# Kernel optimization log

Hardware: AMD Instinct MI355X
Metric: run time of the kernel (lower is better)

Reference implementation:

```python
import jax, jax.numpy as jnp
import numpy as np

N = 50000      # total nodes (actors) across batch
E = 300000     # edges surviving the distance threshold
N_AGT = 128    # n_actor
N_CTX = 128    # n_ctx == n_actor for A2A
EPS = 1e-5


def _gn(x, gamma, beta):
    # torch GroupNorm(num_groups=1) on a [N, C] tensor: normalize over C per row
    mu = jnp.mean(x, axis=-1, keepdims=True)
    var = jnp.mean((x - mu) ** 2, axis=-1, keepdims=True)
    return (x - mu) * jax.lax.rsqrt(var + EPS) * gamma + beta


def setup_inputs() -> dict:
    key = jax.random.key(0)
    ks = jax.random.split(key, 16)
    s = 0.02
    f32 = jnp.float32
    inp = {
        'agts': jax.random.normal(ks[0], (N, N_AGT), f32),
        'ctx': jax.random.normal(ks[1], (N, N_CTX), f32),
        'agt_ctrs': jax.random.normal(ks[2], (N, 2), f32),
        'ctx_ctrs': jax.random.normal(ks[3], (N, 2), f32),
        'hi': jax.random.randint(ks[4], (E,), 0, N, dtype=jnp.int32),
        'wi': jax.random.randint(ks[5], (E,), 0, N, dtype=jnp.int32),
        # dist: nn.Linear(2, n_ctx) -> ReLU -> Linear(n_ctx, n_ctx, GN, act)
        'w_d1': jax.random.normal(ks[6], (N_CTX, 2), f32) * s,
        'b_d1': jnp.zeros((N_CTX,), f32),
        'w_d2': jax.random.normal(ks[7], (N_CTX, N_CTX), f32) * s,
        'g_d2': jnp.ones((N_CTX,), f32), 'bt_d2': jnp.zeros((N_CTX,), f32),
        # query: Linear(n_agt, n_ctx, GN, act)
        'w_q': jax.random.normal(ks[8], (N_CTX, N_AGT), f32) * s,
        'g_q': jnp.ones((N_CTX,), f32), 'bt_q': jnp.zeros((N_CTX,), f32),
        # ctx: Linear(3*n_ctx, n_agt, GN, act) -> nn.Linear(n_agt, n_agt, bias=False)
        'w_c1': jax.random.normal(ks[9], (N_AGT, 3 * N_CTX), f32) * s,
        'g_c1': jnp.ones((N_AGT,), f32), 'bt_c1': jnp.zeros((N_AGT,), f32),
        'w_c2': jax.random.normal(ks[10], (N_AGT, N_AGT), f32) * s,
        # agt: nn.Linear(n_agt, n_agt, bias=False)
        'w_a': jax.random.normal(ks[11], (N_AGT, N_AGT), f32) * s,
        # norm: GroupNorm(1, n_agt)
        'g_n': jnp.ones((N_AGT,), f32), 'bt_n': jnp.zeros((N_AGT,), f32),
        # linear: Linear(n_agt, n_agt, GN, act=False)
        'w_l': jax.random.normal(ks[12], (N_AGT, N_AGT), f32) * s,
        'g_l': jnp.ones((N_AGT,), f32), 'bt_l': jnp.zeros((N_AGT,), f32),
    }
    return inp


def reference(agts, ctx, agt_ctrs, ctx_ctrs, hi, wi,
              w_d1, b_d1, w_d2, g_d2, bt_d2,
              w_q, g_q, bt_q,
              w_c1, g_c1, bt_c1, w_c2,
              w_a, g_n, bt_n,
              w_l, g_l, bt_l):
    res = agts
    # edge-wise distance features: [E, 2] -> [E, n_ctx]
    d = agt_ctrs[hi] - ctx_ctrs[wi]
    d = jax.nn.relu(d @ w_d1.T + b_d1)
    d = jax.nn.relu(_gn(d @ w_d2.T, g_d2, bt_d2))
    # edge-wise query from gathered target nodes: [E, n_ctx]
    q = jax.nn.relu(_gn(agts[hi] @ w_q.T, g_q, bt_q))
    # fuse dist/query/context: [E, 3*n_ctx] -> [E, n_agt]
    e = jnp.concatenate([d, q, ctx[wi]], axis=-1)
    e = jax.nn.relu(_gn(e @ w_c1.T, g_c1, bt_c1))
    e = e @ w_c2.T
    # scatter-add messages back to nodes
    out = agts @ w_a.T
    out = out.at[hi].add(e)
    out = jax.nn.relu(_gn(out, g_n, bt_n))
    out = _gn(out @ w_l.T, g_l, bt_l)
    return jax.nn.relu(out + res)
```

## Files before the change

### kernel.cpp

```cpp
#include <hip/hip_runtime.h>
#include <hip/hip_bf16.h>

#define NCH 128
#define EB  64
#define NB  32

typedef __attribute__((ext_vector_type(8))) short bf16x8;
typedef __attribute__((ext_vector_type(4))) float f32x4;

__device__ inline unsigned short f2bf(float v) {
    __hip_bfloat16 h = __float2bfloat16(v);
    return __builtin_bit_cast(unsigned short, h);
}
__device__ inline float bf2f(unsigned short u) {
    return __builtin_bit_cast(float, (unsigned int)u << 16);
}

__device__ inline bf16x8 cvt8(const float* __restrict__ p) {
    bf16x8 r;
#pragma unroll
    for (int i = 0; i < 8; ++i) r[i] = (short)f2bf(p[i]);
    return r;
}

template<bool BF>
__device__ inline bf16x8 load_row8(const void* __restrict__ src, int node, int koff) {
    if constexpr (BF)
        return *(const bf16x8*)((const unsigned short*)src + (size_t)node * NCH + koff);
    else
        return cvt8((const float*)src + (size_t)node * NCH + koff);
}

__global__ __launch_bounds__(256) void convert_weights_kernel(
    const float* __restrict__ w_d2, const float* __restrict__ w_q,
    const float* __restrict__ w_c1, const float* __restrict__ w_c2,
    const float* __restrict__ w_a,  const float* __restrict__ w_l,
    unsigned short* __restrict__ out)
{
    int i = blockIdx.x * 256 + threadIdx.x;
    if (i >= 131072) return;
    const float* src; int off;
    if      (i < 16384)  { src = w_d2; off = i; }
    else if (i < 32768)  { src = w_q;  off = i - 16384; }
    else if (i < 49152)  { int j = i - 32768; src = w_c1; off = (j >> 7) * 384 + (j & 127); }
    else if (i < 65536)  { int j = i - 49152; src = w_c1; off = (j >> 7) * 384 + 128 + (j & 127); }
    else if (i < 81920)  { int j = i - 65536; src = w_c1; off = (j >> 7) * 384 + 256 + (j & 127); }
    else if (i < 98304)  { src = w_c2; off = i - 81920; }
    else if (i < 114688) { src = w_a;  off = i - 98304; }
    else                 { src = w_l;  off = i - 114688; }
    out[i] = f2bf(src[off]);
}

__device__ inline void gemm_k128_lds(const unsigned short* __restrict__ A,
                                     const unsigned short* __restrict__ W,
                                     int lane, int wave, f32x4 (&acc)[2][2])
{
#pragma unroll
    for (int k = 0; k < 4; ++k) {
        const int koff = k * 32 + (lane >> 4) * 8;
        bf16x8 a[2], b[2];
#pragma unroll
        for (int m = 0; m < 2; ++m) {
            int r = m * 16 + (lane & 15);
            int byte = (r * 256 + koff * 2) ^ ((r & 7) << 4);
            a[m] = *(const bf16x8*)((const char*)A + byte);
        }
#pragma unroll
        for (int n = 0; n < 2; ++n) {
            int wr = wave * 32 + n * 16 + (lane & 15);
            b[n] = *(const bf16x8*)(W + (size_t)wr * NCH + koff);
        }
#pragma unroll
        for (int m = 0; m < 2; ++m)
#pragma unroll
            for (int n = 0; n < 2; ++n)
                acc[m][n] = __builtin_amdgcn_mfma_f32_16x16x32_bf16(a[m], b[n], acc[m][n], 0, 0, 0);
    }
}

__device__ inline void gemm_k128_dual(const unsigned short* __restrict__ A,
                                      const unsigned short* __restrict__ W,
                                      int lane, int wave,
                                      f32x4 (&accA)[2][2], f32x4 (&accB)[2][2])
{
#pragma unroll
    for (int k = 0; k < 4; ++k) {
        const int koff = k * 32 + (lane >> 4) * 8;
        bf16x8 b[2];
#pragma unroll
        for (int n = 0; n < 2; ++n) {
            int wr = wave * 32 + n * 16 + (lane & 15);
            b[n] = *(const bf16x8*)(W + (size_t)wr * NCH + koff);
        }
        bf16x8 a0[2], a1[2];
#pragma unroll
        for (int m = 0; m < 2; ++m) {
            int r = m * 16 + (lane & 15);
            a0[m] = *(const bf16x8*)((const char*)A + ((r * 256 + koff * 2) ^ ((r & 7) << 4)));
            int r2 = r + 32;
            a1[m] = *(const bf16x8*)((const char*)A + ((r2 * 256 + koff * 2) ^ ((r2 & 7) << 4)));
        }
#pragma unroll
        for (int m = 0; m < 2; ++m)
#pragma unroll
            for (int n = 0; n < 2; ++n) {
                accA[m][n] = __builtin_amdgcn_mfma_f32_16x16x32_bf16(a0[m], b[n], accA[m][n], 0, 0, 0);
                accB[m][n] = __builtin_amdgcn_mfma_f32_16x16x32_bf16(a1[m], b[n], accB[m][n], 0, 0, 0);
            }
    }
}

__device__ inline void gn_stats_half(const f32x4 (&acc)[2][2],
                                     float (*red_s)[4], float (*red_q)[4],
                                     int lane, int wave, int roff)
{
#pragma unroll
    for (int m = 0; m < 2; ++m)
#pragma unroll
        for (int j = 0; j < 4; ++j) {
            float sv = acc[m][0][j] + acc[m][1][j];
            float qv = acc[m][0][j] * acc[m][0][j] + acc[m][1][j] * acc[m][1][j];
#pragma unroll
            for (int off = 1; off < 16; off <<= 1) {
                sv += __shfl_xor(sv, off);
                qv += __shfl_xor(qv, off);
            }
            if ((lane & 15) == 0) {
                int r = roff + m * 16 + (lane >> 4) * 4 + j;
                red_s[r][wave] = sv;
                red_q[r][wave] = qv;
            }
        }
}

__device__ inline void gn_apply_half(const f32x4 (&acc)[2][2],
                                     float (*red_s)[4], float (*red_q)[4],
                                     const float* __restrict__ gamma,
                                     const float* __restrict__ beta,
                                     unsigned short* __restrict__ dst,
                                     int lane, int wave, int roff)
{
    const int c0 = wave * 32 + (lane & 15);
    const float g0 = gamma[c0],      b0 = beta[c0];
    const float g1 = gamma[c0 + 16], b1 = beta[c0 + 16];
#pragma unroll
    for (int m = 0; m < 2; ++m)
#pragma unroll
        for (int j = 0; j < 4; ++j) {
            int r = roff + m * 16 + ((lane >> 4) << 2) + j;
            float4 sv = *(const float4*)red_s[r];
            float4 qv = *(const float4*)red_q[r];
            float ssum = (sv.x + sv.y) + (sv.z + sv.w);
            float qsum = (qv.x + qv.y) + (qv.z + qv.w);
            float mu  = ssum * (1.f / NCH);
            float var = qsum * (1.f / NCH) - mu * mu;
            float rs  = rsqrtf(var + 1e-5f);
            float v0 = fmaxf((acc[m][0][j] - mu) * rs * g0 + b0, 0.f);
            float v1 = fmaxf((acc[m][1][j] - mu) * rs * g1 + b1, 0.f);
            unsigned int p0 = f2bf(v0), p1 = f2bf(v1);
            unsigned int o0 = (unsigned int)__shfl_xor((int)p0, 1);
            unsigned int o1 = (unsigned int)__shfl_xor((int)p1, 1);
            if (!(lane & 1)) {
                int cb = c0 * 2;
                int byte0 = (r * 256 + cb) ^ ((r & 7) << 4);
                int byte1 = (r * 256 + cb + 32) ^ ((r & 7) << 4);
                *(unsigned int*)((char*)dst + byte0) = (p0 & 0xffffu) | (o0 << 16);
                *(unsigned int*)((char*)dst + byte1) = (p1 & 0xffffu) | (o1 << 16);
            }
        }
}

__device__ inline void scatter_half(const f32x4 (&acc)[2][2], const int* __restrict__ sh_h,
                                    float* __restrict__ outbuf, int e0, int E,
                                    int lane, int wave, int roff)
{
#pragma unroll
    for (int m = 0; m < 2; ++m)
#pragma unroll
        for (int n = 0; n < 2; ++n)
#pragma unroll
            for (int j = 0; j < 4; ++j) {
                int r = roff + m * 16 + ((lane >> 4) << 2) + j;
                if (e0 + r < E)
                    atomicAdd(&outbuf[(size_t)sh_h[r] * NCH + wave * 32 + n * 16 + (lane & 15)],
                              acc[m][n][j]);
            }
}

__device__ inline void gn_frag_stats(const f32x4 (&acc)[2][2],
                                     float (*red_s)[4], float (*red_q)[4],
                                     int t, float (&mu)[2][4], float (&rs)[2][4])
{
    const int lane = t & 63, wave = t >> 6;
    gn_stats_half(acc, red_s, red_q, lane, wave, 0);
    __syncthreads();
#pragma unroll
    for (int m = 0; m < 2; ++m)
#pragma unroll
        for (int j = 0; j < 4; ++j) {
            int r = m * 16 + ((lane >> 4) << 2) + j;
            float4 sv = *(const float4*)red_s[r];
            float4 qv = *(const float4*)red_q[r];
            float ssum = (sv.x + sv.y) + (sv.z + sv.w);
            float qsum = (qv.x + qv.y) + (qv.z + qv.w);
            float m_  = ssum * (1.f / NCH);
            float var = qsum * (1.f / NCH) - m_ * m_;
            mu[m][j] = m_;
            rs[m][j] = rsqrtf(var + 1e-5f);
        }
}

__device__ inline void gn_pack_store(const f32x4 (&acc)[2][2],
                                     const float (&mu)[2][4], const float (&rs)[2][4],
                                     const float* __restrict__ gamma,
                                     const float* __restrict__ beta,
                                     unsigned short* __restrict__ dst, int t)
{
    const int lane = t & 63, wave = t >> 6;
    const int c0 = wave * 32 + (lane & 15);
    const float g0 = gamma[c0],      b0 = beta[c0];
    const float g1 = gamma[c0 + 16], b1 = beta[c0 + 16];
#pragma unroll
    for (int m = 0; m < 2; ++m)
#pragma unroll
        for (int j = 0; j < 4; ++j) {
            int r = m * 16 + ((lane >> 4) << 2) + j;
            float v0 = fmaxf((acc[m][0][j] - mu[m][j]) * rs[m][j] * g0 + b0, 0.f);
            float v1 = fmaxf((acc[m][1][j] - mu[m][j]) * rs[m][j] * g1 + b1, 0.f);
            unsigned int p0 = f2bf(v0), p1 = f2bf(v1);
            unsigned int o0 = (unsigned int)__shfl_xor((int)p0, 1);
            unsigned int o1 = (unsigned int)__shfl_xor((int)p1, 1);
            if (!(lane & 1)) {
                int cb = c0 * 2;
                int byte0 = (r * 256 + cb) ^ ((r & 7) << 4);
                int byte1 = (r * 256 + cb + 32) ^ ((r & 7) << 4);
                *(unsigned int*)((char*)dst + byte0) = (p0 & 0xffffu) | (o0 << 16);
                *(unsigned int*)((char*)dst + byte1) = (p1 & 0xffffu) | (o1 << 16);
            }
        }
    __syncthreads();
}

__device__ inline void frag_pack_global(const f32x4 (&acc)[2][2],
                                        unsigned short* __restrict__ dst,
                                        int n0, int N, int t)
{
    const int lane = t & 63, wave = t >> 6;
    const int c0 = wave * 32 + (lane & 15);
#pragma unroll
    for (int m = 0; m < 2; ++m)
#pragma unroll
        for (int j = 0; j < 4; ++j) {
            int r = m * 16 + ((lane >> 4) << 2) + j;
            int ng = n0 + r;
            unsigned int p0 = f2bf(acc[m][0][j]);
            unsigned int p1 = f2bf(acc[m][1][j]);
            unsigned int o0 = (unsigned int)__shfl_xor((int)p0, 1);
            unsigned int o1 = (unsigned int)__shfl_xor((int)p1, 1);
            if (!(lane & 1) && ng < N) {
                unsigned int* rowp = (unsigned int*)(dst + (size_t)ng * NCH);
                rowp[c0 >> 1]        = (p0 & 0xffffu) | (o0 << 16);
                rowp[(c0 + 16) >> 1] = (p1 & 0xffffu) | (o1 << 16);
            }
        }
}

__global__ __launch_bounds__(256) void node_prep_kernel(
    const float* __restrict__ agts, const float* __restrict__ ctx,
    const unsigned short* __restrict__ wbf,
    const float* __restrict__ g_q, const float* __restrict__ bt_q,
    float* __restrict__ outbuf,
    unsigned short* __restrict__ pq, unsigned short* __restrict__ px, int N)
{
    const int t = threadIdx.x;
    const int lane = t & 63, wave = t >> 6;
    const int n0 = blockIdx.x * NB;

    __shared__ unsigned short bfQ[NB * NCH];
    __shared__ __align__(16) float red_s[NB][4];
    __shared__ __align__(16) float red_q[NB][4];

    const unsigned short* Wq   = wbf + 16384;
    const unsigned short* Wc1q = wbf + 49152;
    const unsigned short* Wc1x = wbf + 65536;
    const unsigned short* Wa   = wbf + 98304;

    int r0 = n0 + (lane & 15);      if (r0 >= N) r0 = N - 1;
    int r1 = n0 + 16 + (lane & 15); if (r1 >= N) r1 = N - 1;

    const f32x4 z = { 0.f, 0.f, 0.f, 0.f };
    f32x4 accO[2][2] = { { z, z }, { z, z } };
    f32x4 accQ[2][2] = { { z, z }, { z, z } };
#pragma unroll
    for (int k = 0; k < 4; ++k) {
        const int koff = k * 32 + (lane >> 4) * 8;
        bf16x8 a[2], bo[2], bq[2];
        a[0] = load_row8<false>(agts, r0, koff);
        a[1] = load_row8<false>(agts, r1, koff);
#pragma unroll
        for (int n = 0; n < 2; ++n) {
            int wr = wave * 32 + n * 16 + (lane & 15);
            bo[n] = *(const bf16x8*)(Wa + (size_t)wr * NCH + koff);
            bq[n] = *(const bf16x8*)(Wq + (size_t)wr * NCH + koff);
        }
#pragma unroll
        for (int m = 0; m < 2; ++m)
#pragma unroll
            for (int n = 0; n < 2; ++n) {
                accO[m][n] = __builtin_amdgcn_mfma_f32_16x16x32_bf16(a[m], bo[n], accO[m][n], 0, 0, 0);
                accQ[m][n] = __builtin_amdgcn_mfma_f32_16x16x32_bf16(a[m], bq[n], accQ[m][n], 0, 0, 0);
            }
    }
#pragma unroll
    for (int m = 0; m < 2; ++m)
#pragma unroll
        for (int n = 0; n < 2; ++n)
#pragma unroll
            for (int j = 0; j < 4; ++j) {
                int r = m * 16 + ((lane >> 4) << 2) + j;
                int ng = n0 + r;
                if (ng < N)
                    outbuf[(size_t)ng * NCH + wave * 32 + n * 16 + (lane & 15)] = accO[m][n][j];
            }
    float mu[2][4], rs[2][4];
    gn_frag_stats(accQ, red_s, red_q, t, mu, rs);
    gn_pack_store(accQ, mu, rs, g_q, bt_q, bfQ, t);

    f32x4 accPq[2][2] = { { z, z }, { z, z } };
    f32x4 accPx[2][2] = { { z, z }, { z, z } };
#pragma unroll
    for (int k = 0; k < 4; ++k) {
        const int koff = k * 32 + (lane >> 4) * 8;
        bf16x8 aq[2], ax[2], bq2[2], bx[2];
#pragma unroll
        for (int m = 0; m < 2; ++m) {
            int r = m * 16 + (lane & 15);
            int byte = (r * 256 + koff * 2) ^ ((r & 7) << 4);
            aq[m] = *(const bf16x8*)((const char*)bfQ + byte);
        }
        ax[0] = load_row8<false>(ctx, r0, koff);
        ax[1] = load_row8<false>(ctx, r1, koff);
#pragma unroll
        for (int n = 0; n < 2; ++n) {
            int wr = wave * 32 + n * 16 + (lane & 15);
            bq2[n] = *(const bf16x8*)(Wc1q + (size_t)wr * NCH + koff);
            bx[n]  = *(const bf16x8*)(Wc1x + (size_t)wr * NCH + koff);
        }
#pragma unroll
        for (int m = 0; m < 2; ++m)
#pragma unroll
            for (int n = 0; n < 2; ++n) {
                accPq[m][n] = __builtin_amdgcn_mfma_f32_16x16x32_bf16(aq[m], bq2[n], accPq[m][n], 0, 0, 0);
                accPx[m][n] = __builtin_amdgcn_mfma_f32_16x16x32_bf16(ax[m], bx[n], accPx[m][n], 0, 0, 0);
            }
    }
    frag_pack_global(accPq, pq, n0, N, t);
    frag_pack_global(accPx, px, n0, N, t);
}

__global__ __launch_bounds__(256) void edge_kernel_pre(
    const unsigned short* __restrict__ pq, const unsigned short* __restrict__ px,
    const float* __restrict__ agt_ctrs, const float* __restrict__ ctx_ctrs,
    const int* __restrict__ hi, const int* __restrict__ wi,
    const float* __restrict__ w_d1, const float* __restrict__ b_d1,
    const float* __restrict__ g_d2, const float* __restrict__ bt_d2,
    const float* __restrict__ g_c1, const float* __restrict__ bt_c1,
    const unsigned short* __restrict__ wbf,
    float* __restrict__ outbuf, int E)
{
    const int t = threadIdx.x;
    const int lane = t & 63;
    const int wave = t >> 6;
    const int e0 = blockIdx.x * EB;

    __shared__ unsigned short bfD[EB * NCH];
    __shared__ float S[EB][NCH + 4];
    __shared__ __align__(16) float red_s[EB][4];
    __shared__ __align__(16) float red_q[EB][4];
    __shared__ int   sh_h[EB], sh_w[EB];
    __shared__ float sh_dx[EB], sh_dy[EB];

    const unsigned short* Wd2  = wbf;
    const unsigned short* Wc1d = wbf + 32768;
    const unsigned short* Wc2  = wbf + 81920;

    if (t < EB) {
        int e = e0 + t; if (e >= E) e = E - 1;
        int h = hi[e], w = wi[e];
        sh_h[t] = h; sh_w[t] = w;
        sh_dx[t] = agt_ctrs[2 * h]     - ctx_ctrs[2 * w];
        sh_dy[t] = agt_ctrs[2 * h + 1] - ctx_ctrs[2 * w + 1];
    }
    __syncthreads();

    {
        const int r  = t >> 2;
        const int q4 = t & 3;
        const int h = sh_h[r], w = sh_w[r];
#pragma unroll
        for (int i = 0; i < 4; ++i) {
            int c8 = (q4 * 4 + i) * 8;
            bf16x8 aq = load_row8<true>(pq, h, c8);
            bf16x8 ax = load_row8<true>(px, w, c8);
            float4 lo, hi4;
            lo.x = bf2f((unsigned short)aq[0]) + bf2f((unsigned short)ax[0]);
            lo.y = bf2f((unsigned short)aq[1]) + bf2f((unsigned short)ax[1]);
            lo.z = bf2f((unsigned short)aq[2]) + bf2f((unsigned short)ax[2]);
            lo.w = bf2f((unsigned short)aq[3]) + bf2f((unsigned short)ax[3]);
            hi4.x = bf2f((unsigned short)aq[4]) + bf2f((unsigned short)ax[4]);
            hi4.y = bf2f((unsigned short)aq[5]) + bf2f((unsigned short)ax[5]);
            hi4.z = bf2f((unsigned short)aq[6]) + bf2f((unsigned short)ax[6]);
            hi4.w = bf2f((unsigned short)aq[7]) + bf2f((unsigned short)ax[7]);
            *(float4*)&S[r][c8]     = lo;
            *(float4*)&S[r][c8 + 4] = hi4;
        }
    }
    {
        const int c = t & 127, rh = t >> 7;
        const float wa = w_d1[2 * c], wb = w_d1[2 * c + 1], bb = b_d1[c];
#pragma unroll
        for (int i = 0; i < 32; ++i) {
            int r = rh * 32 + i;
            float v = fmaxf(fmaf(wa, sh_dx[r], fmaf(wb, sh_dy[r], bb)), 0.f);
            unsigned int pv = f2bf(v);
            unsigned int ov = (unsigned int)__shfl_xor((int)pv, 1);
            if (!(c & 1)) {
                int byte = (r * 256 + c * 2) ^ ((r & 7) << 4);
                *(unsigned int*)((char*)bfD + byte) = (pv & 0xffffu) | (ov << 16);
            }
        }
    }
    __syncthreads();

    const f32x4 z = { 0.f, 0.f, 0.f, 0.f };
    f32x4 accA[2][2], accB[2][2];

    accA[0][0] = z; accA[0][1] = z; accA[1][0] = z; accA[1][1] = z;
    accB[0][0] = z; accB[0][1] = z; accB[1][0] = z; accB[1][1] = z;
    gemm_k128_dual(bfD, Wd2, lane, wave, accA, accB);
    gn_stats_half(accA, red_s, red_q, lane, wave, 0);
    gn_stats_half(accB, red_s, red_q, lane, wave, 32);
    __syncthreads();
    gn_apply_half(accA, red_s, red_q, g_d2, bt_d2, bfD, lane, wave, 0);
    gn_apply_half(accB, red_s, red_q, g_d2, bt_d2, bfD, lane, wave, 32);
    __syncthreads();

    {
        const int c0 = wave * 32 + (lane & 15);
#pragma unroll
        for (int m = 0; m < 2; ++m)
#pragma unroll
            for (int j = 0; j < 4; ++j) {
                int r = m * 16 + ((lane >> 4) << 2) + j;
                accA[m][0][j] = S[r][c0];      accA[m][1][j] = S[r][c0 + 16];
                accB[m][0][j] = S[r + 32][c0]; accB[m][1][j] = S[r + 32][c0 + 16];
            }
    }
    gemm_k128_dual(bfD, Wc1d, lane, wave, accA, accB);
    gn_stats_half(accA, red_s, red_q, lane, wave, 0);
    gn_stats_half(accB, red_s, red_q, lane, wave, 32);
    __syncthreads();
    gn_apply_half(accA, red_s, red_q, g_c1, bt_c1, bfD, lane, wave, 0);
    gn_apply_half(accB, red_s, red_q, g_c1, bt_c1, bfD, lane, wave, 32);
    __syncthreads();

    accA[0][0] = z; accA[0][1] = z; accA[1][0] = z; accA[1][1] = z;
    accB[0][0] = z; accB[0][1] = z; accB[1][0] = z; accB[1][1] = z;
    gemm_k128_dual(bfD, Wc2, lane, wave, accA, accB);
    scatter_half(accA, sh_h, outbuf, e0, E, lane, wave, 0);
    scatter_half(accB, sh_h, outbuf, e0, E, lane, wave, 32);
}

__global__ __launch_bounds__(256) void edge_kernel_fb(
    const float* __restrict__ agts, const float* __restrict__ ctx,
    const float* __restrict__ agt_ctrs, const float* __restrict__ ctx_ctrs,
    const int* __restrict__ hi, const int* __restrict__ wi,
    const float* __restrict__ w_d1, const float* __restrict__ b_d1,
    const float* __restrict__ g_d2, const float* __restrict__ bt_d2,
    const float* __restrict__ g_q, const float* __restrict__ bt_q,
    const float* __restrict__ g_c1, const float* __restrict__ bt_c1,
    const unsigned short* __restrict__ wbf,
    float* __restrict__ outbuf, int E)
{
    const int t = threadIdx.x;
    const int lane = t & 63;
    const int wave = t >> 6;
    const int e0 = blockIdx.x * 32;

    __shared__ unsigned short bfQ[32 * NCH];
    __shared__ unsigned short bfD[32 * NCH];
    __shared__ unsigned short bfX[32 * NCH];
    __shared__ __align__(16) float red_s[32][4];
    __shared__ __align__(16) float red_q[32][4];
    __shared__ int   sh_h[32], sh_w[32];
    __shared__ float sh_dx[32], sh_dy[32];

    const unsigned short* Wd2 = wbf;
    const unsigned short* Wq  = wbf + 16384;
    const unsigned short* Wc1d = wbf + 32768;
    const unsigned short* Wc1q = wbf + 49152;
    const unsigned short* Wc1x = wbf + 65536;
    const unsigned short* Wc2 = wbf + 81920;

    if (t < 32) {
        int e = e0 + t; if (e >= E) e = E - 1;
        int h = hi[e], w = wi[e];
        sh_h[t] = h; sh_w[t] = w;
        sh_dx[t] = agt_ctrs[2 * h]     - ctx_ctrs[2 * w];
        sh_dy[t] = agt_ctrs[2 * h + 1] - ctx_ctrs[2 * w + 1];
    }
    __syncthreads();
    {
        const int r  = t >> 3;
        const int cc = t & 7;
        const int h = sh_h[r], w = sh_w[r];
#pragma unroll
        for (int half = 0; half < 2; ++half) {
            int c = cc + half * 8;
            bf16x8 qv = load_row8<false>(agts, h, c * 8);
            bf16x8 xv = load_row8<false>(ctx, w, c * 8);
            int byte = (r * 256 + c * 16) ^ ((r & 7) << 4);
            *(bf16x8*)((char*)bfQ + byte) = qv;
            *(bf16x8*)((char*)bfX + byte) = xv;
        }
    }
    {
        const int c = t & 127, rh = t >> 7;
        const float wa = w_d1[2 * c], wb = w_d1[2 * c + 1], bb = b_d1[c];
#pragma unroll
        for (int i = 0; i < 16; ++i) {
            int r = rh * 16 + i;
            float v = fmaxf(fmaf(wa, sh_dx[r], fmaf(wb, sh_dy[r], bb)), 0.f);
            unsigned int pv = f2bf(v);
            unsigned int ov = (unsigned int)__shfl_xor((int)pv, 1);
            if (!(c & 1)) {
                int byte = (r * 256 + c * 2) ^ ((r & 7) << 4);
                *(unsigned int*)((char*)bfD + byte) = (pv & 0xffffu) | (ov << 16);
            }
        }
    }
    __syncthreads();

    const f32x4 z = { 0.f, 0.f, 0.f, 0.f };
    f32x4 acc[2][2];
    float mu[2][4], rs[2][4];

    acc[0][0] = z; acc[0][1] = z; acc[1][0] = z; acc[1][1] = z;
    gemm_k128_lds(bfD, Wd2, lane, wave, acc);
    gn_frag_stats(acc, red_s, red_q, t, mu, rs);
    gn_pack_store(acc, mu, rs, g_d2, bt_d2, bfD, t);

    acc[0][0] = z; acc[0][1] = z; acc[1][0] = z; acc[1][1] = z;
    gemm_k128_lds(bfQ, Wq, lane, wave, acc);
    gn_frag_stats(acc, red_s, red_q, t, mu, rs);
    gn_pack_store(acc, mu, rs, g_q, bt_q, bfQ, t);

    acc[0][0] = z; acc[0][1] = z; acc[1][0] = z; acc[1][1] = z;
    gemm_k128_lds(bfD, Wc1d, lane, wave, acc);
    gemm_k128_lds(bfQ, Wc1q, lane, wave, acc);
    gemm_k128_lds(bfX, Wc1x, lane, wave, acc);
    gn_frag_stats(acc, red_s, red_q, t, mu, rs);
    gn_pack_store(acc, mu, rs, g_c1, bt_c1, bfD, t);

    acc[0][0] = z; acc[0][1] = z; acc[1][0] = z; acc[1][1] = z;
    gemm_k128_lds(bfD, Wc2, lane, wave, acc);
#pragma unroll
    for (int m = 0; m < 2; ++m)
#pragma unroll
        for (int n = 0; n < 2; ++n)
#pragma unroll
            for (int j = 0; j < 4; ++j) {
                int r = m * 16 + ((lane >> 4) << 2) + j;
                if (e0 + r < E)
                    atomicAdd(&outbuf[(size_t)sh_h[r] * NCH + wave * 32 + n * 16 + (lane & 15)],
                              acc[m][n][j]);
            }
}

__global__ __launch_bounds__(256) void node_init_kernel(
    const float* __restrict__ agts, const unsigned short* __restrict__ wa_bf,
    float* __restrict__ outbuf, int N)
{
    const int t = threadIdx.x;
    const int lane = t & 63, wave = t >> 6;
    const int n0 = blockIdx.x * NB;

    int r0 = n0 + (lane & 15);      if (r0 >= N) r0 = N - 1;
    int r1 = n0 + 16 + (lane & 15); if (r1 >= N) r1 = N - 1;

    const f32x4 z = { 0.f, 0.f, 0.f, 0.f };
    f32x4 acc[2][2] = { { z, z }, { z, z } };
#pragma unroll
    for (int k = 0; k < 4; ++k) {
        const int koff = k * 32 + (lane >> 4) * 8;
        bf16x8 a[2], b[2];
        a[0] = load_row8<false>(agts, r0, koff);
        a[1] = load_row8<false>(agts, r1, koff);
#pragma unroll
        for (int n = 0; n < 2; ++n) {
            int wr = wave * 32 + n * 16 + (lane & 15);
            b[n] = *(const bf16x8*)(wa_bf + (size_t)wr * NCH + koff);
        }
#pragma unroll
        for (int m = 0; m < 2; ++m)
#pragma unroll
            for (int n = 0; n < 2; ++n)
                acc[m][n] = __builtin_amdgcn_mfma_f32_16x16x32_bf16(a[m], b[n], acc[m][n], 0, 0, 0);
    }
#pragma unroll
    for (int m = 0; m < 2; ++m)
#pragma unroll
        for (int n = 0; n < 2; ++n)
#pragma unroll
            for (int j = 0; j < 4; ++j) {
                int r = m * 16 + ((lane >> 4) << 2) + j;
                int ng = n0 + r;
                if (ng < N)
                    outbuf[(size_t)ng * NCH + wave * 32 + n * 16 + (lane & 15)] = acc[m][n][j];
            }
}

__global__ __launch_bounds__(256) void node_post_kernel(
    float* __restrict__ outbuf, const float* __restrict__ agts,
    const float* __restrict__ g_n, const float* __restrict__ bt_n,
    const unsigned short* __restrict__ wl_bf,
    const float* __restrict__ g_l, const float* __restrict__ bt_l, int N)
{
    const int t = threadIdx.x;
    const int lane = t & 63, wave = t >> 6;
    const int n0 = blockIdx.x * NB;

    __shared__ unsigned short bfP[NB * NCH];
    __shared__ __align__(16) float red_s[NB][4];
    __shared__ __align__(16) float red_q[NB][4];

    const int c = t & 127, rh = t >> 7;
    float v[16];
#pragma unroll
    for (int i = 0; i < 16; ++i) {
        int n = n0 + rh * 16 + i; if (n >= N) n = N - 1;
        v[i] = outbuf[(size_t)n * NCH + c];
    }
#pragma unroll
    for (int i = 0; i < 16; ++i) {
        float s = v[i], q = v[i] * v[i];
        for (int off = 32; off > 0; off >>= 1) {
            s += __shfl_down(s, off);
            q += __shfl_down(q, off);
        }
        if (lane == 0) { red_s[rh * 16 + i][wave & 1] = s; red_q[rh * 16 + i][wave & 1] = q; }
    }
    __syncthreads();
    {
        const float g = g_n[c], b = bt_n[c];
#pragma unroll
        for (int i = 0; i < 16; ++i) {
            int r = rh * 16 + i;
            float s = red_s[r][0] + red_s[r][1];
            float q = red_q[r][0] + red_q[r][1];
            float m_  = s * (1.f / NCH);
            float var = q * (1.f / NCH) - m_ * m_;
            float rrs = rsqrtf(var + 1e-5f);
            float val = fmaxf((v[i] - m_) * rrs * g + b, 0.f);
            unsigned int pv = f2bf(val);
            unsigned int ov = (unsigned int)__shfl_xor((int)pv, 1);
            if (!(c & 1)) {
                int byte = (r * 256 + c * 2) ^ ((r & 7) << 4);
                *(unsigned int*)((char*)bfP + byte) = (pv & 0xffffu) | (ov << 16);
            }
        }
    }
    __syncthreads();

    const f32x4 z = { 0.f, 0.f, 0.f, 0.f };
    f32x4 acc[2][2] = { { z, z }, { z, z } };
    gemm_k128_lds(bfP, wl_bf, lane, wave, acc);

    float mu[2][4], rs[2][4];
    gn_frag_stats(acc, red_s, red_q, t, mu, rs);
    const int c0 = wave * 32 + (lane & 15);
    const float g0 = g_l[c0],      b0 = bt_l[c0];
    const float g1 = g_l[c0 + 16], b1 = bt_l[c0 + 16];
#pragma unroll
    for (int m = 0; m < 2; ++m)
#pragma unroll
        for (int j = 0; j < 4; ++j) {
            int r = m * 16 + ((lane >> 4) << 2) + j;
            int ng = n0 + r;
            if (ng < N) {
                float v0 = (acc[m][0][j] - mu[m][j]) * rs[m][j] * g0 + b0;
                float v1 = (acc[m][1][j] - mu[m][j]) * rs[m][j] * g1 + b1;
                v0 = fmaxf(v0 + agts[(size_t)ng * NCH + c0], 0.f);
                v1 = fmaxf(v1 + agts[(size_t)ng * NCH + c0 + 16], 0.f);
                outbuf[(size_t)ng * NCH + c0]      = v0;
                outbuf[(size_t)ng * NCH + c0 + 16] = v1;
            }
        }
}

extern "C" void kernel_launch(void* const* d_in, const int* in_sizes, int n_in,
                              void* d_out, int out_size, void* d_ws, size_t ws_size,
                              hipStream_t stream) {
    const float* agts     = (const float*)d_in[0];
    const float* ctx      = (const float*)d_in[1];
    const float* agt_ctrs = (const float*)d_in[2];
    const float* ctx_ctrs = (const float*)d_in[3];
    const int*   hi       = (const int*)d_in[4];
    const int*   wi       = (const int*)d_in[5];
    const float* w_d1     = (const float*)d_in[6];
    const float* b_d1     = (const float*)d_in[7];
    const float* w_d2     = (const float*)d_in[8];
    const float* g_d2     = (const float*)d_in[9];
    const float* bt_d2    = (const float*)d_in[10];
    const float* w_q      = (const float*)d_in[11];
    const float* g_q      = (const float*)d_in[12];
    const float* bt_q     = (const float*)d_in[13];
    const float* w_c1     = (const float*)d_in[14];
    const float* g_c1     = (const float*)d_in[15];
    const float* bt_c1    = (const float*)d_in[16];
    const float* w_c2     = (const float*)d_in[17];
    const float* w_a      = (const float*)d_in[18];
    const float* g_n      = (const float*)d_in[19];
    const float* bt_n     = (const float*)d_in[20];
    const float* w_l      = (const float*)d_in[21];
    const float* g_l      = (const float*)d_in[22];
    const float* bt_l     = (const float*)d_in[23];

    const int N = in_sizes[0] / NCH;
    const int E = in_sizes[4];

    float* outbuf = (float*)d_out;

    unsigned short* wbf = (unsigned short*)d_ws;
    unsigned short* pq  = wbf + 131072;
    unsigned short* px  = pq + (size_t)N * NCH;
    const size_t need = 262144ull + (size_t)N * NCH * 4ull;
    const bool big = (d_ws != nullptr) && (ws_size >= need);

    const int nb_nodes = (N + NB - 1) / NB;

    convert_weights_kernel<<<512, 256, 0, stream>>>(w_d2, w_q, w_c1, w_c2, w_a, w_l, wbf);

    if (big) {
        node_prep_kernel<<<nb_nodes, 256, 0, stream>>>(
            agts, ctx, wbf, g_q, bt_q, outbuf, pq, px, N);
        edge_kernel_pre<<<(E + EB - 1) / EB, 256, 0, stream>>>(
            pq, px, agt_ctrs, ctx_ctrs, hi, wi,
            w_d1, b_d1, g_d2, bt_d2, g_c1, bt_c1,
            wbf, outbuf, E);
    } else {
        node_init_kernel<<<nb_nodes, 256, 0, stream>>>(agts, wbf + 98304, outbuf, N);
        edge_kernel_fb<<<(E + 31) / 32, 256, 0, stream>>>(
            agts, ctx, agt_ctrs, ctx_ctrs, hi, wi,
            w_d1, b_d1, g_d2, bt_d2, g_q, bt_q, g_c1, bt_c1,
            wbf, outbuf, E);
    }
    node_post_kernel<<<nb_nodes, 256, 0, stream>>>(
        outbuf, agts, g_n, bt_n, wbf + 114688, g_l, bt_l, N);
}
```

Measured before the change: 305.4 us.

## Move c2 projection after scatter and accumulate edges with packed bf16 atomics

Since w_c2 is linear, the per-edge c2 GEMM is moved past the scatter-add: edges scatter their GN+ReLU activations into a bf16 node buffer, and a new node kernel applies w_c2 once per node before the final norm/linear stages. The scatter uses global_atomic_pk_add_bf16 on packed pairs, halving atomic count and bytes versus fp32 atomics. This removes one E-sized GEMM and replaces it with an N-sized one, but accumulating in bf16 loses precision for high-degree nodes and adds a memset plus extra workspace.

```diff
diff --git a/kernel.cpp b/kernel.cpp
--- a/kernel.cpp
+++ b/kernel.cpp
@@ -29,6 +29,11 @@
         return *(const bf16x8*)((const unsigned short*)src + (size_t)node * NCH + koff);
     else
         return cvt8((const float*)src + (size_t)node * NCH + koff);
+}
+
+__device__ inline void pk_add_bf16(unsigned short* dst, unsigned int packed) {
+    unsigned long long a = (unsigned long long)dst;
+    asm volatile("global_atomic_pk_add_bf16 %0, %1, off" :: "v"(a), "v"(packed) : "memory");
 }
 
 __global__ __launch_bounds__(256) void convert_weights_kernel(
@@ -170,21 +175,40 @@
         }
 }
 
-__device__ inline void scatter_half(const f32x4 (&acc)[2][2], const int* __restrict__ sh_h,
-                                    float* __restrict__ outbuf, int e0, int E,
-                                    int lane, int wave, int roff)
-{
-#pragma unroll
-    for (int m = 0; m < 2; ++m)
-#pragma unroll
-        for (int n = 0; n < 2; ++n)
-#pragma unroll
-            for (int j = 0; j < 4; ++j) {
-                int r = roff + m * 16 + ((lane >> 4) << 2) + j;
-                if (e0 + r < E)
-                    atomicAdd(&outbuf[(size_t)sh_h[r] * NCH + wave * 32 + n * 16 + (lane & 15)],
-                              acc[m][n][j]);
-            }
+__device__ inline void gn_scatter_half(const f32x4 (&acc)[2][2],
+                                       float (*red_s)[4], float (*red_q)[4],
+                                       const float* __restrict__ gamma,
+                                       const float* __restrict__ beta,
+                                       const int* __restrict__ sh_h,
+                                       unsigned short* __restrict__ out,
+                                       int e0, int E, int lane, int wave, int roff)
+{
+    const int c0 = wave * 32 + (lane & 15);
+    const float g0 = gamma[c0],      b0 = beta[c0];
+    const float g1 = gamma[c0 + 16], b1 = beta[c0 + 16];
+#pragma unroll
+    for (int m = 0; m < 2; ++m)
+#pragma unroll
+        for (int j = 0; j < 4; ++j) {
+            int r = roff + m * 16 + ((lane >> 4) << 2) + j;
+            float4 sv = *(const float4*)red_s[r];
+            float4 qv = *(const float4*)red_q[r];
+            float ssum = (sv.x + sv.y) + (sv.z + sv.w);
+            float qsum = (qv.x + qv.y) + (qv.z + qv.w);
+            float mu  = ssum * (1.f / NCH);
+            float var = qsum * (1.f / NCH) - mu * mu;
+            float rs  = rsqrtf(var + 1e-5f);
+            float v0 = fmaxf((acc[m][0][j] - mu) * rs * g0 + b0, 0.f);
+            float v1 = fmaxf((acc[m][1][j] - mu) * rs * g1 + b1, 0.f);
+            unsigned int p0 = f2bf(v0), p1 = f2bf(v1);
+            unsigned int o0 = (unsigned int)__shfl_xor((int)p0, 1);
+            unsigned int o1 = (unsigned int)__shfl_xor((int)p1, 1);
+            if (!(lane & 1) && e0 + r < E) {
+                unsigned short* rowp = out + (size_t)sh_h[r] * NCH;
+                pk_add_bf16(rowp + c0,      (p0 & 0xffffu) | (o0 << 16));
+                pk_add_bf16(rowp + c0 + 16, (p1 & 0xffffu) | (o1 << 16));
+            }
+        }
 }
 
 __device__ inline void gn_frag_stats(const f32x4 (&acc)[2][2],
@@ -269,7 +293,7 @@
     const float* __restrict__ agts, const float* __restrict__ ctx,
     const unsigned short* __restrict__ wbf,
     const float* __restrict__ g_q, const float* __restrict__ bt_q,
-    float* __restrict__ outbuf,
+    float* __restrict__ basebuf,
     unsigned short* __restrict__ pq, unsigned short* __restrict__ px, int N)
 {
     const int t = threadIdx.x;
@@ -320,7 +344,7 @@
                 int r = m * 16 + ((lane >> 4) << 2) + j;
                 int ng = n0 + r;
                 if (ng < N)
-                    outbuf[(size_t)ng * NCH + wave * 32 + n * 16 + (lane & 15)] = accO[m][n][j];
+                    basebuf[(size_t)ng * NCH + wave * 32 + n * 16 + (lane & 15)] = accO[m][n][j];
             }
     float mu[2][4], rs[2][4];
     gn_frag_stats(accQ, red_s, red_q, t, mu, rs);
@@ -358,7 +382,7 @@
     frag_pack_global(accPx, px, n0, N, t);
 }
 
-__global__ __launch_bounds__(256) void edge_kernel_pre(
+__global__ __launch_bounds__(256) void edge_kernel_pk(
     const unsigned short* __restrict__ pq, const unsigned short* __restrict__ px,
     const float* __restrict__ agt_ctrs, const float* __restrict__ ctx_ctrs,
     const int* __restrict__ hi, const int* __restrict__ wi,
@@ -366,7 +390,7 @@
     const float* __restrict__ g_d2, const float* __restrict__ bt_d2,
     const float* __restrict__ g_c1, const float* __restrict__ bt_c1,
     const unsigned short* __restrict__ wbf,
-    float* __restrict__ outbuf, int E)
+    unsigned short* __restrict__ c1sum, int E)
 {
     const int t = threadIdx.x;
     const int lane = t & 63;
@@ -382,7 +406,6 @@
 
     const unsigned short* Wd2  = wbf;
     const unsigned short* Wc1d = wbf + 32768;
-    const unsigned short* Wc2  = wbf + 81920;
 
     if (t < EB) {
         int e = e0 + t; if (e >= E) e = E - 1;
@@ -460,15 +483,85 @@
     gn_stats_half(accA, red_s, red_q, lane, wave, 0);
     gn_stats_half(accB, red_s, red_q, lane, wave, 32);
     __syncthreads();
-    gn_apply_half(accA, red_s, red_q, g_c1, bt_c1, bfD, lane, wave, 0);
-    gn_apply_half(accB, red_s, red_q, g_c1, bt_c1, bfD, lane, wave, 32);
-    __syncthreads();
-
-    accA[0][0] = z; accA[0][1] = z; accA[1][0] = z; accA[1][1] = z;
-    accB[0][0] = z; accB[0][1] = z; accB[1][0] = z; accB[1][1] = z;
-    gemm_k128_dual(bfD, Wc2, lane, wave, accA, accB);
-    scatter_half(accA, sh_h, outbuf, e0, E, lane, wave, 0);
-    scatter_half(accB, sh_h, outbuf, e0, E, lane, wave, 32);
+    gn_scatter_half(accA, red_s, red_q, g_c1, bt_c1, sh_h, c1sum, e0, E, lane, wave, 0);
+    gn_scatter_half(accB, red_s, red_q, g_c1, bt_c1, sh_h, c1sum, e0, E, lane, wave, 32);
+}
+
+__global__ __launch_bounds__(256) void node_post_c2_kernel(
+    const unsigned short* __restrict__ c1sum, float* __restrict__ dst,
+    const float* __restrict__ agts,
+    const float* __restrict__ g_n, const float* __restrict__ bt_n,
+    const unsigned short* __restrict__ wc2_bf, const unsigned short* __restrict__ wl_bf,
+    const float* __restrict__ g_l, const float* __restrict__ bt_l, int N)
+{
+    const int t = threadIdx.x;
+    const int lane = t & 63, wave = t >> 6;
+    const int n0 = blockIdx.x * NB;
+
+    __shared__ unsigned short bfP[NB * NCH];
+    __shared__ __align__(16) float red_s[NB][4];
+    __shared__ __align__(16) float red_q[NB][4];
+
+    int r0 = n0 + (lane & 15);      if (r0 >= N) r0 = N - 1;
+    int r1 = n0 + 16 + (lane & 15); if (r1 >= N) r1 = N - 1;
+
+    const f32x4 z = { 0.f, 0.f, 0.f, 0.f };
+    f32x4 acc[2][2] = { { z, z }, { z, z } };
+#pragma unroll
+    for (int k = 0; k < 4; ++k) {
+        const int koff = k * 32 + (lane >> 4) * 8;
+        bf16x8 a[2], b[2];
+        a[0] = load_row8<true>(c1sum, r0, koff);
+        a[1] = load_row8<true>(c1sum, r1, koff);
+#pragma unroll
+        for (int n = 0; n < 2; ++n) {
+            int wr = wave * 32 + n * 16 + (lane & 15);
+            b[n] = *(const bf16x8*)(wc2_bf + (size_t)wr * NCH + koff);
+        }
+#pragma unroll
+        for (int m = 0; m < 2; ++m)
+#pragma unroll
+            for (int n = 0; n < 2; ++n)
+                acc[m][n] = __builtin_amdgcn_mfma_f32_16x16x32_bf16(a[m], b[n], acc[m][n], 0, 0, 0);
+    }
+#pragma unroll
+    for (int m = 0; m < 2; ++m)
+#pragma unroll
+        for (int n = 0; n < 2; ++n)
+#pragma unroll
+            for (int j = 0; j < 4; ++j) {
+                int r = m * 16 + ((lane >> 4) << 2) + j;
+                int ng = n0 + r;
+                if (ng < N)
+                    acc[m][n][j] += dst[(size_t)ng * NCH + wave * 32 + n * 16 + (lane & 15)];
+            }
+
+    float mu[2][4], rs[2][4];
+    gn_frag_stats(acc, red_s, red_q, t, mu, rs);
+    gn_pack_store(acc, mu, rs, g_n, bt_n, bfP, t);
+
+    f32x4 acc2[2][2] = { { z, z }, { z, z } };
+    gemm_k128_lds(bfP, wl_bf, lane, wave, acc2);
+
+    gn_frag_stats(acc2, red_s, red_q, t, mu, rs);
+    const int c0 = wave * 32 + (lane & 15);
+    const float g0 = g_l[c0],      b0 = bt_l[c0];
+    const float g1 = g_l[c0 + 16], b1 = bt_l[c0 + 16];
+#pragma unroll
+    for (int m = 0; m < 2; ++m)
+#pragma unroll
+        for (int j = 0; j < 4; ++j) {
+            int r = m * 16 + ((lane >> 4) << 2) + j;
+            int ng = n0 + r;
+            if (ng < N) {
+                float v0 = (acc2[m][0][j] - mu[m][j]) * rs[m][j] * g0 + b0;
+                float v1 = (acc2[m][1][j] - mu[m][j]) * rs[m][j] * g1 + b1;
+                v0 = fmaxf(v0 + agts[(size_t)ng * NCH + c0], 0.f);
+                v1 = fmaxf(v1 + agts[(size_t)ng * NCH + c0 + 16], 0.f);
+                dst[(size_t)ng * NCH + c0]      = v0;
+                dst[(size_t)ng * NCH + c0 + 16] = v1;
+            }
+        }
 }
 
 __global__ __launch_bounds__(256) void edge_kernel_fb(
@@ -620,8 +713,8 @@
             }
 }
 
-__global__ __launch_bounds__(256) void node_post_kernel(
-    float* __restrict__ outbuf, const float* __restrict__ agts,
+__global__ __launch_bounds__(256) void node_post_fb_kernel(
+    float* __restrict__ dst, const float* __restrict__ agts,
     const float* __restrict__ g_n, const float* __restrict__ bt_n,
     const unsigned short* __restrict__ wl_bf,
     const float* __restrict__ g_l, const float* __restrict__ bt_l, int N)
@@ -639,7 +732,7 @@
 #pragma unroll
     for (int i = 0; i < 16; ++i) {
         int n = n0 + rh * 16 + i; if (n >= N) n = N - 1;
-        v[i] = outbuf[(size_t)n * NCH + c];
+        v[i] = dst[(size_t)n * NCH + c];
     }
 #pragma unroll
     for (int i = 0; i < 16; ++i) {
@@ -692,8 +785,8 @@
                 float v1 = (acc[m][1][j] - mu[m][j]) * rs[m][j] * g1 + b1;
                 v0 = fmaxf(v0 + agts[(size_t)ng * NCH + c0], 0.f);
                 v1 = fmaxf(v1 + agts[(size_t)ng * NCH + c0 + 16], 0.f);
-                outbuf[(size_t)ng * NCH + c0]      = v0;
-                outbuf[(size_t)ng * NCH + c0 + 16] = v1;
+                dst[(size_t)ng * NCH + c0]      = v0;
+                dst[(size_t)ng * NCH + c0 + 16] = v1;
             }
         }
 }
@@ -729,32 +822,37 @@
     const int N = in_sizes[0] / NCH;
     const int E = in_sizes[4];
 
-    float* outbuf = (float*)d_out;
-
-    unsigned short* wbf = (unsigned short*)d_ws;
-    unsigned short* pq  = wbf + 131072;
-    unsigned short* px  = pq + (size_t)N * NCH;
-    const size_t need = 262144ull + (size_t)N * NCH * 4ull;
-    const bool big = (d_ws != nullptr) && (ws_size >= need);
+    float* outf32 = (float*)d_out;
+
+    unsigned short* wbf   = (unsigned short*)d_ws;
+    unsigned short* pq    = wbf + 131072;
+    unsigned short* px    = pq + (size_t)N * NCH;
+    unsigned short* c1sum = px + (size_t)N * NCH;
+    const size_t need_pk = 262144ull + (size_t)N * NCH * 6ull;
+    const bool pk = (d_ws != nullptr) && (ws_size >= need_pk);
 
     const int nb_nodes = (N + NB - 1) / NB;
 
     convert_weights_kernel<<<512, 256, 0, stream>>>(w_d2, w_q, w_c1, w_c2, w_a, w_l, wbf);
 
-    if (big) {
+    if (pk) {
         node_prep_kernel<<<nb_nodes, 256, 0, stream>>>(
-            agts, ctx, wbf, g_q, bt_q, outbuf, pq, px, N);
-        edge_kernel_pre<<<(E + EB - 1) / EB, 256, 0, stream>>>(
+            agts, ctx, wbf, g_q, bt_q, outf32, pq, px, N);
+        hipMemsetAsync(c1sum, 0, (size_t)N * NCH * 2, stream);
+        edge_kernel_pk<<<(E + EB - 1) / EB, 256, 0, stream>>>(
             pq, px, agt_ctrs, ctx_ctrs, hi, wi,
             w_d1, b_d1, g_d2, bt_d2, g_c1, bt_c1,
-            wbf, outbuf, E);
+            wbf, c1sum, E);
+        node_post_c2_kernel<<<nb_nodes, 256, 0, stream>>>(
+            c1sum, outf32, agts, g_n, bt_n,
+            wbf + 81920, wbf + 114688, g_l, bt_l, N);
     } else {
-        node_init_kernel<<<nb_nodes, 256, 0, stream>>>(agts, wbf + 98304, outbuf, N);
+        node_init_kernel<<<nb_nodes, 256, 0, stream>>>(agts, wbf + 98304, outf32, N);
         edge_kernel_fb<<<(E + 31) / 32, 256, 0, stream>>>(
             agts, ctx, agt_ctrs, ctx_ctrs, hi, wi,
             w_d1, b_d1, g_d2, bt_d2, g_q, bt_q, g_c1, bt_c1,
-            wbf, outbuf, E);
-    }
-    node_post_kernel<<<nb_nodes, 256, 0, stream>>>(
-        outbuf, agts, g_n, bt_n, wbf + 114688, g_l, bt_l, N);
-}
+            wbf, outf32, E);
+        node_post_fb_kernel<<<nb_nodes, 256, 0, stream>>>(
+            outf32, agts, g_n, bt_n, wbf + 114688, g_l, bt_l, N);
+    }
+}
```

Result: slower. 328.6 us (+7.6%).
